# Optimization experiments

Hardware: AMD Instinct MI355X
Metric: run time of the kernel (lower is better)

The kernel has to match this reference:

```python
import jax, jax.numpy as jnp
import numpy as np

N = 100000
E = 1600000
F = 128
HID = 64
OUT = 64
LSTM_H = (3 * HID) // 2  # 96, PyG JumpingKnowledge lstm hidden size


def setup_inputs() -> dict:
    key = jax.random.key(0)
    ks = jax.random.split(key, 40)

    def w(k, shape, s=0.05):
        return jax.random.normal(k, shape, dtype=jnp.float32) * s

    inp = {}
    inp['x'] = jax.random.normal(ks[0], (N, F), dtype=jnp.float32)
    inp['edge_index'] = jax.random.randint(ks[1], (2, E), 0, N)
    # GINConv MLPs: Linear(in,hid) -> ReLU -> Linear(hid,hid)
    dims = [(F, HID), (HID, HID), (HID, HID)]
    for i, (a, b) in enumerate(dims):
        inp[f'W{i}a'] = w(ks[2 + 4 * i], (b, a))
        inp[f'b{i}a'] = w(ks[3 + 4 * i], (b,))
        inp[f'W{i}b'] = w(ks[4 + 4 * i], (b, b))
        inp[f'b{i}b'] = w(ks[5 + 4 * i], (b,))
    # JK bidirectional LSTM (torch gate order i,f,g,o)
    for j, d in enumerate(['f', 'b']):
        inp[f'Wih_{d}'] = w(ks[14 + 4 * j], (4 * LSTM_H, HID))
        inp[f'Whh_{d}'] = w(ks[15 + 4 * j], (4 * LSTM_H, LSTM_H))
        inp[f'bih_{d}'] = w(ks[16 + 4 * j], (4 * LSTM_H,))
        inp[f'bhh_{d}'] = w(ks[17 + 4 * j], (4 * LSTM_H,))
    inp['Watt'] = w(ks[22], (1, 2 * LSTM_H))
    inp['batt'] = w(ks[23], (1,))
    inp['Wlin'] = w(ks[24], (OUT, HID))
    inp['blin'] = w(ks[25], (OUT,))
    inp['Wfc1'] = w(ks[26], (1, OUT))
    inp['bfc1'] = w(ks[27], (1,))
    inp['Wfc2'] = w(ks[28], (1, N))
    inp['bfc2'] = w(ks[29], (1,))
    return inp


def _gin_layer(h, src, dst, Wa, ba, Wb, bb):
    # GINConv with eps=0: MLP((1+eps)*x + sum_{j in N(i)} x_j)
    agg = jax.ops.segment_sum(h[src], dst, num_segments=h.shape[0])
    z = h + agg
    z = jnp.maximum(z @ Wa.T + ba, 0.0)
    return z @ Wb.T + bb


def _lstm_scan(seq, Wih, Whh, bih, bhh):
    # seq: [L, N, C]; returns hidden states [L, N, H]
    H = Whh.shape[1]
    bias = bih + bhh

    def cell(carry, xt):
        hp, cp = carry
        g = xt @ Wih.T + hp @ Whh.T + bias
        i, f, gg, o = jnp.split(g, 4, axis=-1)
        c = jax.nn.sigmoid(f) * cp + jax.nn.sigmoid(i) * jnp.tanh(gg)
        hn = jax.nn.sigmoid(o) * jnp.tanh(c)
        return (hn, c), hn

    n = seq.shape[1]
    init = (jnp.zeros((n, H), seq.dtype), jnp.zeros((n, H), seq.dtype))
    _, hs = jax.lax.scan(cell, init, seq)
    return hs


def reference(x, edge_index, W0a, b0a, W0b, b0b, W1a, b1a, W1b, b1b,
              W2a, b2a, W2b, b2b, Wih_f, Whh_f, bih_f, bhh_f,
              Wih_b, Whh_b, bih_b, bhh_b, Watt, batt, Wlin, blin,
              Wfc1, bfc1, Wfc2, bfc2):
    src, dst = edge_index[0], edge_index[1]
    h = x
    xs = []
    for (Wa, ba, Wb, bb) in [(W0a, b0a, W0b, b0b), (W1a, b1a, W1b, b1b),
                             (W2a, b2a, W2b, b2b)]:
        h = _gin_layer(h, src, dst, Wa, ba, Wb, bb)
        h = jnp.maximum(h, 0.0)  # BasicGNN act (relu); dropout=identity in eval
        xs.append(h)
    seq = jnp.stack(xs, axis=0)  # [L, N, HID]
    hf = _lstm_scan(seq, Wih_f, Whh_f, bih_f, bhh_f)
    hb = _lstm_scan(seq[::-1], Wih_b, Whh_b, bih_b, bhh_b)[::-1]
    ao = jnp.concatenate([hf, hb], axis=-1)  # [L, N, 2*LSTM_H]
    alpha = (ao @ Watt.T + batt)[..., 0]  # [L, N]
    alpha = jax.nn.softmax(alpha, axis=0)  # softmax over layers
    xjk = jnp.einsum('lnc,ln->nc', seq, alpha)  # [N, HID]
    xo = xjk @ Wlin.T + blin  # [N, OUT]
    v = (xo @ Wfc1.T + bfc1)[:, 0]  # [N]
    v = jnp.where(v >= 0, v, 0.01 * v)  # LeakyReLU
    return Wfc2 @ v + bfc2  # [1]
```

## Files before the change

kernel.cpp:

```cpp
#include <hip/hip_runtime.h>
#include <stdint.h>

typedef unsigned short u16;
typedef unsigned int u32;
using short8 = __attribute__((ext_vector_type(8))) short;
using f32x16 = __attribute__((ext_vector_type(16))) float;

__device__ __forceinline__ float sigf(float x){
  return __builtin_amdgcn_rcpf(1.0f + __expf(-x));
}
__device__ __forceinline__ float tanh_f(float x){
  return 1.0f - 2.0f*__builtin_amdgcn_rcpf(1.0f + __expf(2.0f*x));
}
__device__ __forceinline__ u16 f2bf(float f){
  u32 u = __float_as_uint(f);
  u += 0x7FFFu + ((u>>16)&1u);
  return (u16)(u>>16);
}
__device__ __forceinline__ float bf2f(u16 h){ return __uint_as_float(((u32)h)<<16); }

__global__ void k_deg(const int* __restrict__ dst, int* __restrict__ deg, int E){
  int i = blockIdx.x*256 + threadIdx.x;
  if (i < E) atomicAdd(&deg[dst[i]], 1);
}

__global__ __launch_bounds__(256) void k_scan1(const int* __restrict__ deg, int* __restrict__ indptr,
                                               int* __restrict__ bsum, int N){
  __shared__ int s[256];
  int tid = threadIdx.x;
  int i = blockIdx.x*256 + tid;
  int v = (i < N) ? deg[i] : 0;
  s[tid] = v; __syncthreads();
  for (int off=1; off<256; off<<=1){
    int t = (tid>=off) ? s[tid-off] : 0;
    __syncthreads();
    s[tid] += t;
    __syncthreads();
  }
  if (i < N) indptr[i] = s[tid] - v;
  if (tid == 255) bsum[blockIdx.x] = s[255];
}

__global__ __launch_bounds__(512) void k_scan2(const int* __restrict__ bsum, int* __restrict__ boffs,
                                               int* __restrict__ indptr, int nb, int N){
  __shared__ int s[512];
  int tid = threadIdx.x;
  int v = (tid < nb) ? bsum[tid] : 0;
  s[tid] = v; __syncthreads();
  for (int off=1; off<512; off<<=1){
    int t = (tid>=off) ? s[tid-off] : 0;
    __syncthreads();
    s[tid] += t;
    __syncthreads();
  }
  boffs[tid] = s[tid] - v;
  if (tid == nb-1) indptr[N] = s[tid];
}

__global__ __launch_bounds__(256) void k_scan3(int* __restrict__ indptr, const int* __restrict__ boffs, int N){
  int i = blockIdx.x*256 + threadIdx.x;
  if (i < N) indptr[i] += boffs[blockIdx.x];
}

__global__ void k_fill(const int* __restrict__ src, const int* __restrict__ dst,
                       const int* __restrict__ indptr, int* __restrict__ fill,
                       int* __restrict__ col, int E){
  int i = blockIdx.x*256 + threadIdx.x;
  if (i < E){
    int d = dst[i];
    int r = atomicAdd(&fill[d], 1);
    col[indptr[d] + r] = src[i];
  }
}

template<int F>
__global__ __launch_bounds__(256) void k_agg(const float* __restrict__ y, const int* __restrict__ indptr,
                                             const int* __restrict__ col, const float* __restrict__ bias,
                                             float* __restrict__ z, int N){
  constexpr int TPN = F/4;
  constexpr int NPB = 256/TPN;
  int n = blockIdx.x*NPB + threadIdx.x/TPN;
  int lane = threadIdx.x % TPN;
  if (n >= N) return;
  const float4* hv = (const float4*)y;
  float4 acc = hv[(size_t)n*TPN + lane];
  int s = indptr[n], e = indptr[n+1];
  int p = s;
  for (; p + 8 <= e; p += 8){
    int c8[8];
    #pragma unroll
    for (int i=0;i<8;++i) c8[i] = col[p+i];
    #pragma unroll
    for (int i=0;i<8;++i){
      float4 x = hv[(size_t)c8[i]*TPN + lane];
      acc.x += x.x; acc.y += x.y; acc.z += x.z; acc.w += x.w;
    }
  }
  for (; p < e; ++p){
    float4 x = hv[(size_t)col[p]*TPN + lane];
    acc.x += x.x; acc.y += x.y; acc.z += x.z; acc.w += x.w;
  }
  float4 b4 = ((const float4*)bias)[lane];
  acc.x = fmaxf(acc.x + b4.x, 0.f);
  acc.y = fmaxf(acc.y + b4.y, 0.f);
  acc.z = fmaxf(acc.z + b4.z, 0.f);
  acc.w = fmaxf(acc.w + b4.w, 0.f);
  ((float4*)z)[(size_t)n*TPN + lane] = acc;
}

__device__ __forceinline__ void packW1_body(int idx, const float* __restrict__ Wih,
                                            const float* __restrict__ Whh, u16* __restrict__ Wp){
  if (idx >= 10*12*64*8) return;
  int i  = idx & 7;
  int l  = (idx>>3) & 63;
  int rt = (idx>>9) % 12;
  int kt = (idx>>9) / 12;
  int r  = rt*32 + (l & 31);
  int j  = r >> 2, g = r & 3;
  int row = g*96 + j;
  int k  = kt*16 + ((l>>5)<<3) + i;
  float v = (k < 64) ? Wih[row*64 + k] : Whh[row*96 + (k-64)];
  Wp[idx] = f2bf(v);
}

__device__ __forceinline__ void packG_body(int idx, const float* __restrict__ W,
                                           u16* __restrict__ Wg, int K){
  if (idx >= K*128) return;
  int i  = idx & 7;
  int l  = (idx>>3) & 63;
  int p  = (idx>>9) & 1;
  int rt = (idx>>10) & 1;
  int kt = idx >> 11;
  int j  = rt*32 + (l & 31);
  int k  = kt*16 + ((l>>5)<<3) + i;
  float v = W[(size_t)j*K + k];
  u16 h = f2bf(v);
  Wg[idx] = p ? f2bf(v - bf2f(h)) : h;
}

__global__ __launch_bounds__(256) void k_packAll(
    const float* __restrict__ Wih_f, const float* __restrict__ Whh_f,
    const float* __restrict__ Wih_b, const float* __restrict__ Whh_b,
    const float* __restrict__ bih_f, const float* __restrict__ bhh_f,
    const float* __restrict__ bih_b, const float* __restrict__ bhh_b,
    const float* __restrict__ W0a, const float* __restrict__ W0b,
    const float* __restrict__ W1a, const float* __restrict__ W1b,
    const float* __restrict__ W2a, const float* __restrict__ W2b,
    const float* __restrict__ Wlin,
    u16* __restrict__ Wpf, u16* __restrict__ Wpb,
    float4* __restrict__ Bpf, float4* __restrict__ Bpb,
    u16* __restrict__ Wg0a, u16* __restrict__ Wg0b,
    u16* __restrict__ Wg1a, u16* __restrict__ Wg1b,
    u16* __restrict__ Wg2a, u16* __restrict__ Wg2b,
    u16* __restrict__ WgL)
{
  int b = blockIdx.x;
  int tid = threadIdx.x;
  if (b < 240){ packW1_body(b*256+tid, Wih_f, Whh_f, Wpf); return; }
  b -= 240;
  if (b < 240){ packW1_body(b*256+tid, Wih_b, Whh_b, Wpb); return; }
  b -= 240;
  if (b == 0){
    if (tid < 96){
      int j = tid;
      Bpf[j] = make_float4(bih_f[j]+bhh_f[j], bih_f[96+j]+bhh_f[96+j],
                           bih_f[192+j]+bhh_f[192+j], bih_f[288+j]+bhh_f[288+j]);
    } else if (tid >= 128 && tid < 224){
      int j = tid - 128;
      Bpb[j] = make_float4(bih_b[j]+bhh_b[j], bih_b[96+j]+bhh_b[96+j],
                           bih_b[192+j]+bhh_b[192+j], bih_b[288+j]+bhh_b[288+j]);
    }
    return;
  }
  b -= 1;
  if (b < 64){ packG_body(b*256+tid, W0a, Wg0a, 128); return; }
  b -= 64;
  if (b < 32){ packG_body(b*256+tid, W0b, Wg0b, 64); return; }
  b -= 32;
  if (b < 32){ packG_body(b*256+tid, W1a, Wg1a, 64); return; }
  b -= 32;
  if (b < 32){ packG_body(b*256+tid, W1b, Wg1b, 64); return; }
  b -= 32;
  if (b < 32){ packG_body(b*256+tid, W2a, Wg2a, 64); return; }
  b -= 32;
  if (b < 32){ packG_body(b*256+tid, W2b, Wg2b, 64); return; }
  b -= 32;
  packG_body(b*256+tid, Wlin, WgL, 64);
}

__device__ __forceinline__ void cvt8p(const float (&v)[8], u32 (&hw)[4], u32 (&lw)[4]){
  #pragma unroll
  for (int i=0;i<4;++i){
    u16 h0=f2bf(v[2*i]),   h1=f2bf(v[2*i+1]);
    u16 l0=f2bf(v[2*i]-bf2f(h0)), l1=f2bf(v[2*i+1]-bf2f(h1));
    hw[i]= (u32)h0 | ((u32)h1<<16);
    lw[i]= (u32)l0 | ((u32)l1<<16);
  }
}

__device__ __forceinline__ void stageG(const float (&v)[8], u16* __restrict__ BH, u16* __restrict__ BL,
                                       int node, int kc, int NKT){
  u32 hw[4], lw[4];
  cvt8p(v, hw, lw);
  int kt = kc >> 1, h2 = kc & 1;
  int sl = (((h2<<5) | (node&31)) ^ (kc & 7));
  int addr = (((node>>5)*NKT + kt)<<9) + (sl<<3);
  *(uint4*)(BH + addr) = make_uint4(hw[0],hw[1],hw[2],hw[3]);
  *(uint4*)(BL + addr) = make_uint4(lw[0],lw[1],lw[2],lw[3]);
}

template<int K, int ACT>
__global__ __launch_bounds__(256,2) void k_mfgemm(const float* __restrict__ A, const u16* __restrict__ Wg,
                                                  const float* __restrict__ bias, float* __restrict__ out,
                                                  int N){
  constexpr int NKT = K/16;
  __shared__ u16 BH[2*NKT*512];
  __shared__ u16 BL[2*NKT*512];
  const int tid = threadIdx.x;
  const int l = tid & 63;
  const int w = __builtin_amdgcn_readfirstlane(tid >> 6);
  const int rt = w >> 1, nt = w & 1;
  const int nb = blockIdx.x * 64;
  const int hi = l >> 5;

  for (int u = tid; u < 64*(K/8); u += 256){
    int node = u / (K/8);
    int kc = u % (K/8);
    int n = nb + node;
    float v[8];
    if (n < N){
      const float4* s4 = (const float4*)(A + (size_t)n*K + kc*8);
      float4 a = s4[0], b = s4[1];
      v[0]=a.x; v[1]=a.y; v[2]=a.z; v[3]=a.w; v[4]=b.x; v[5]=b.y; v[6]=b.z; v[7]=b.w;
    } else {
      #pragma unroll
      for (int i=0;i<8;++i) v[i]=0.f;
    }
    stageG(v, BH, BL, node, kc, NKT);
  }
  __syncthreads();

  f32x16 acc;
  #pragma unroll
  for (int r=0;r<16;++r) acc[r] = 0.f;
  const u16* wbase = Wg + ((size_t)rt<<10) + ((size_t)l<<3);
  #pragma unroll
  for (int kt = 0; kt < NKT; ++kt){
    const u16* wk = wbase + (size_t)kt*2048;
    short8 Ah = *(const short8*)(wk);
    short8 Al = *(const short8*)(wk + 512);
    int sl = l ^ (((kt<<1) + hi) & 7);
    int baddr = ((nt*NKT + kt)<<9) + (sl<<3);
    short8 Bh = *(const short8*)(BH + baddr);
    short8 Bl = *(const short8*)(BL + baddr);
    acc = __builtin_amdgcn_mfma_f32_32x32x16_bf16(Ah, Bh, acc, 0,0,0);
    acc = __builtin_amdgcn_mfma_f32_32x32x16_bf16(Ah, Bl, acc, 0,0,0);
    acc = __builtin_amdgcn_mfma_f32_32x32x16_bf16(Al, Bh, acc, 0,0,0);
  }

  const int col = l & 31;
  const int n = nb + nt*32 + col;
  if (n < N){
    #pragma unroll
    for (int g = 0; g < 4; ++g){
      const int j0 = rt*32 + 8*g + 4*hi;
      float4 b4 = bias ? *(const float4*)(bias + j0) : make_float4(0.f,0.f,0.f,0.f);
      float4 o;
      o.x = acc[4*g+0] + b4.x;
      o.y = acc[4*g+1] + b4.y;
      o.z = acc[4*g+2] + b4.z;
      o.w = acc[4*g+3] + b4.w;
      if (ACT){
        o.x = fmaxf(o.x, 0.f); o.y = fmaxf(o.y, 0.f);
        o.z = fmaxf(o.z, 0.f); o.w = fmaxf(o.w, 0.f);
      }
      *(float4*)(out + (size_t)n*64 + j0) = o;
    }
  }
}

__global__ __launch_bounds__(256,2) void k_mfgemm2(const float* __restrict__ Z, const u16* __restrict__ Wgb,
                                                   const float* __restrict__ bb, const u16* __restrict__ Wga,
                                                   float* __restrict__ Hout, float* __restrict__ Yout,
                                                   int N){
  __shared__ u16 BH[4096];
  __shared__ u16 BL[4096];
  __shared__ float hX[64][68];
  const int tid = threadIdx.x;
  const int l = tid & 63;
  const int w = __builtin_amdgcn_readfirstlane(tid >> 6);
  const int rt = w >> 1, nt = w & 1;
  const int nb = blockIdx.x * 64;
  const int hi = l >> 5;
  const int col = l & 31;
  const int n = nb + nt*32 + col;

  for (int u = tid; u < 512; u += 256){
    int node = u >> 3;
    int kc = u & 7;
    int nn = nb + node;
    float v[8];
    if (nn < N){
      const float4* s4 = (const float4*)(Z + (size_t)nn*64 + kc*8);
      float4 a = s4[0], b = s4[1];
      v[0]=a.x; v[1]=a.y; v[2]=a.z; v[3]=a.w; v[4]=b.x; v[5]=b.y; v[6]=b.z; v[7]=b.w;
    } else {
      #pragma unroll
      for (int i=0;i<8;++i) v[i]=0.f;
    }
    stageG(v, BH, BL, node, kc, 4);
  }
  __syncthreads();

  f32x16 acc;
  #pragma unroll
  for (int r=0;r<16;++r) acc[r] = 0.f;
  {
    const u16* wbase = Wgb + ((size_t)rt<<10) + ((size_t)l<<3);
    #pragma unroll
    for (int kt = 0; kt < 4; ++kt){
      const u16* wk = wbase + (size_t)kt*2048;
      short8 Ah = *(const short8*)(wk);
      short8 Al = *(const short8*)(wk + 512);
      int sl = l ^ (((kt<<1) + hi) & 7);
      int baddr = ((nt*4 + kt)<<9) + (sl<<3);
      short8 Bh = *(const short8*)(BH + baddr);
      short8 Bl = *(const short8*)(BL + baddr);
      acc = __builtin_amdgcn_mfma_f32_32x32x16_bf16(Ah, Bh, acc, 0,0,0);
      acc = __builtin_amdgcn_mfma_f32_32x32x16_bf16(Ah, Bl, acc, 0,0,0);
      acc = __builtin_amdgcn_mfma_f32_32x32x16_bf16(Al, Bh, acc, 0,0,0);
    }
  }
  {
    const int node = nt*32 + col;
    #pragma unroll
    for (int g = 0; g < 4; ++g){
      const int j0 = rt*32 + 8*g + 4*hi;
      float4 b4 = *(const float4*)(bb + j0);
      float4 o;
      o.x = fmaxf(acc[4*g+0] + b4.x, 0.f);
      o.y = fmaxf(acc[4*g+1] + b4.y, 0.f);
      o.z = fmaxf(acc[4*g+2] + b4.z, 0.f);
      o.w = fmaxf(acc[4*g+3] + b4.w, 0.f);
      if (n < N) *(float4*)(Hout + (size_t)n*64 + j0) = o;
      *(float4*)(&hX[node][j0]) = o;
    }
  }
  __syncthreads();

  for (int u = tid; u < 512; u += 256){
    int node = u >> 3;
    int kc = u & 7;
    float v[8];
    #pragma unroll
    for (int i=0;i<8;++i) v[i] = hX[node][kc*8 + i];
    stageG(v, BH, BL, node, kc, 4);
  }
  __syncthreads();

  #pragma unroll
  for (int r=0;r<16;++r) acc[r] = 0.f;
  {
    const u16* wbase = Wga + ((size_t)rt<<10) + ((size_t)l<<3);
    #pragma unroll
    for (int kt = 0; kt < 4; ++kt){
      const u16* wk = wbase + (size_t)kt*2048;
      short8 Ah = *(const short8*)(wk);
      short8 Al = *(const short8*)(wk + 512);
      int sl = l ^ (((kt<<1) + hi) & 7);
      int baddr = ((nt*4 + kt)<<9) + (sl<<3);
      short8 Bh = *(const short8*)(BH + baddr);
      short8 Bl = *(const short8*)(BL + baddr);
      acc = __builtin_amdgcn_mfma_f32_32x32x16_bf16(Ah, Bh, acc, 0,0,0);
      acc = __builtin_amdgcn_mfma_f32_32x32x16_bf16(Ah, Bl, acc, 0,0,0);
      acc = __builtin_amdgcn_mfma_f32_32x32x16_bf16(Al, Bh, acc, 0,0,0);
    }
  }
  if (n < N){
    #pragma unroll
    for (int g = 0; g < 4; ++g){
      const int j0 = rt*32 + 8*g + 4*hi;
      float4 o;
      o.x = acc[4*g+0]; o.y = acc[4*g+1]; o.z = acc[4*g+2]; o.w = acc[4*g+3];
      *(float4*)(Yout + (size_t)n*64 + j0) = o;
    }
  }
}

__device__ __forceinline__ void ldx_regs(const float* __restrict__ seq, int blk, int N, int tid,
                                         float (&v)[8]){
  int node = tid >> 3;
  int kc = tid & 7;
  int n = blk*32 + node;
  if (n < N){
    const float4* s4 = (const float4*)(seq + (size_t)n*64 + kc*8);
    float4 a = s4[0], b = s4[1];
    v[0]=a.x; v[1]=a.y; v[2]=a.z; v[3]=a.w; v[4]=b.x; v[5]=b.y; v[6]=b.z; v[7]=b.w;
  } else {
    #pragma unroll
    for (int i=0;i<8;++i) v[i]=0.f;
  }
}

__device__ __forceinline__ void stage_x_h16(const float (&v)[8], u16* __restrict__ XH, int tid){
  int node = tid >> 3;
  int kc = tid & 7;
  u32 hw[4];
  #pragma unroll
  for (int i=0;i<4;++i)
    hw[i] = (u32)f2bf(v[2*i]) | ((u32)f2bf(v[2*i+1])<<16);
  int kt = kc >> 1, hi = kc & 1;
  int sl = (((hi<<5) | node) ^ (kc & 7));
  int addr = (kt<<9) + (sl<<3);
  *(uint4*)(XH + addr) = make_uint4(hw[0],hw[1],hw[2],hw[3]);
}

__device__ __forceinline__ void restage_h16(const u16 (*hFH)[32], u16* __restrict__ XH, int tid){
  int node = tid & 31;
  #pragma unroll
  for (int q = 0; q < 2; ++q){
    int cc = (tid >> 5) + q*8;
    if (cc < 12){
      int kth = cc >> 1, hi = cc & 1;
      int ktG = kth + 4;
      u32 hw[4];
      #pragma unroll
      for (int i=0;i<4;++i){
        u16 a = hFH[cc*8 + 2*i][node];
        u16 b = hFH[cc*8 + 2*i + 1][node];
        hw[i] = (u32)a | ((u32)b<<16);
      }
      int sl = (((hi<<5) | node) ^ ((2*ktG + hi) & 7));
      int addr = (ktG<<9) + (sl<<3);
      *(uint4*)(XH + addr) = make_uint4(hw[0],hw[1],hw[2],hw[3]);
    }
  }
}

template<int FIRST, int WRITEH>
__device__ __forceinline__ float lstm_step5(const u16* __restrict__ Wp,
    const float4* __restrict__ Bp, const float* __restrict__ WattW,
    const u16* __restrict__ XH, u16 (*hFH)[32],
    float (&c)[12], int rtg, int l)
{
  constexpr int NKT = FIRST ? 4 : 10;
  const int hi = l >> 5;
  const int col = l & 31;
  f32x16 acc[3];
  #pragma unroll
  for (int t=0;t<3;++t)
    #pragma unroll
    for (int r=0;r<16;++r) acc[t][r] = 0.f;

  const u16* wbase = Wp + (size_t)(rtg*3)*512 + ((size_t)l<<3);
  #pragma unroll
  for (int kt = 0; kt < NKT; ++kt){
    const u16* wk = wbase + (size_t)kt*6144;
    short8 A0 = *(const short8*)(wk);
    short8 A1 = *(const short8*)(wk + 512);
    short8 A2 = *(const short8*)(wk + 1024);
    int sl = l ^ (((kt<<1) + hi) & 7);
    int baddr = (kt<<9) + (sl<<3);
    short8 Bh = *(const short8*)(XH + baddr);
    __builtin_amdgcn_s_setprio(1);
    acc[0] = __builtin_amdgcn_mfma_f32_32x32x16_bf16(A0, Bh, acc[0], 0,0,0);
    acc[1] = __builtin_amdgcn_mfma_f32_32x32x16_bf16(A1, Bh, acc[1], 0,0,0);
    acc[2] = __builtin_amdgcn_mfma_f32_32x32x16_bf16(A2, Bh, acc[2], 0,0,0);
    __builtin_amdgcn_s_setprio(0);
  }

  float aP = 0.f;
  #pragma unroll
  for (int ti=0;ti<3;++ti){
    #pragma unroll
    for (int rg=0; rg<4; ++rg){
      const int j = (rtg*3+ti)*8 + 2*rg + hi;
      float4 bv = Bp[j];
      float gi = acc[ti][rg*4+0] + bv.x;
      float gf = acc[ti][rg*4+1] + bv.y;
      float gg = acc[ti][rg*4+2] + bv.z;
      float go = acc[ti][rg*4+3] + bv.w;
      const int ci = ti*4 + rg;
      float cp = FIRST ? 0.f : c[ci];
      float cn = sigf(gf)*cp + sigf(gi)*tanh_f(gg);
      float hh = sigf(go)*tanh_f(cn);
      c[ci] = cn;
      aP = fmaf(hh, WattW[j], aP);
      if (WRITEH) hFH[j][col] = f2bf(hh);
    }
  }
  return aP;
}

__global__ __launch_bounds__(256,2) void k_lstm5(
    const float* __restrict__ h1, const float* __restrict__ h2, const float* __restrict__ h3,
    const u16* __restrict__ Wpf, const u16* __restrict__ Wpb,
    const float4* __restrict__ Bpf, const float4* __restrict__ Bpb,
    const float* __restrict__ Watt, const float* __restrict__ batt,
    float* __restrict__ aF, float* __restrict__ aB, int gL, int N)
{
  __shared__ u16 XH[5120];
  __shared__ u16 hFH[96][32];
  __shared__ float sAl[4][3][32];
  const int tid = threadIdx.x;
  const int l = tid & 63;
  const int rtg = __builtin_amdgcn_readfirstlane(tid >> 6);
  const int dir = (blockIdx.x >= gL) ? 1 : 0;
  const int blk = blockIdx.x - dir*gL;
  const float* sA = dir ? h3 : h1;
  const float* sC = dir ? h1 : h3;
  const u16* Wp = dir ? Wpb : Wpf;
  const float4* Bp = dir ? Bpb : Bpf;
  const float* WattW = Watt + dir*96;
  float* aD = dir ? aB : aF;
  float c[12];
  float a0, a1, a2;
  float xv[8];

  ldx_regs(sA, blk, N, tid, xv);
  stage_x_h16(xv, XH, tid);
  ldx_regs(h2, blk, N, tid, xv);
  __syncthreads();

  a0 = lstm_step5<1,1>(Wp, Bp, WattW, XH, hFH, c, rtg, l);
  __syncthreads();
  stage_x_h16(xv, XH, tid);
  restage_h16(hFH, XH, tid);
  ldx_regs(sC, blk, N, tid, xv);
  __syncthreads();

  a1 = lstm_step5<0,1>(Wp, Bp, WattW, XH, hFH, c, rtg, l);
  __syncthreads();
  stage_x_h16(xv, XH, tid);
  restage_h16(hFH, XH, tid);
  __syncthreads();

  a2 = lstm_step5<0,0>(Wp, Bp, WattW, XH, hFH, c, rtg, l);

  a0 += __shfl_xor(a0, 32);
  a1 += __shfl_xor(a1, 32);
  a2 += __shfl_xor(a2, 32);
  if (l < 32){
    sAl[rtg][0][l] = a0;
    sAl[rtg][1][l] = a1;
    sAl[rtg][2][l] = a2;
  }
  __syncthreads();
  if (tid < 96){
    int s = tid >> 5;
    int node = tid & 31;
    int n = blk*32 + node;
    if (n < N){
      float sum = sAl[0][s][node] + sAl[1][s][node]
                + sAl[2][s][node] + sAl[3][s][node];
      int slice = dir ? (2 - s) : s;
      float v = dir ? sum : (batt[0] + sum);
      aD[(size_t)slice*N + n] = v;
    }
  }
}

__global__ __launch_bounds__(256,2) void k_jk2(const float* __restrict__ aF, const float* __restrict__ aB,
                                               const float* __restrict__ h1, const float* __restrict__ h2,
                                               const float* __restrict__ h3,
                                               const u16* __restrict__ WgL, const float* __restrict__ blin,
                                               const float* __restrict__ Wfc1, const float* __restrict__ bfc1,
                                               float* __restrict__ vout, int N){
  __shared__ u16 BH[4096];
  __shared__ u16 BL[4096];
  __shared__ float sP[4][32];
  const int tid = threadIdx.x;
  const int l = tid & 63;
  const int w = __builtin_amdgcn_readfirstlane(tid >> 6);
  const int rt = w >> 1, nt = w & 1;
  const int nb = blockIdx.x * 64;
  const int hi = l >> 5;

  for (int u = tid; u < 512; u += 256){
    int node = u >> 3;
    int kc = u & 7;
    int n = nb + node;
    float v[8];
    if (n < N){
      float a0 = aF[n] + aB[n];
      float a1 = aF[(size_t)N + n] + aB[(size_t)N + n];
      float a2 = aF[(size_t)2*N + n] + aB[(size_t)2*N + n];
      float m = fmaxf(a0, fmaxf(a1, a2));
      float e0 = __expf(a0-m), e1 = __expf(a1-m), e2 = __expf(a2-m);
      float inv = __builtin_amdgcn_rcpf(e0+e1+e2);
      float w0 = e0*inv, w1 = e1*inv, w2 = e2*inv;
      const float4* p1 = (const float4*)(h1 + (size_t)n*64 + kc*8);
      const float4* p2 = (const float4*)(h2 + (size_t)n*64 + kc*8);
      const float4* p3 = (const float4*)(h3 + (size_t)n*64 + kc*8);
      #pragma unroll
      for (int q=0;q<2;++q){
        float4 x1 = p1[q], x2 = p2[q], x3 = p3[q];
        v[4*q+0] = w0*x1.x + w1*x2.x + w2*x3.x;
        v[4*q+1] = w0*x1.y + w1*x2.y + w2*x3.y;
        v[4*q+2] = w0*x1.z + w1*x2.z + w2*x3.z;
        v[4*q+3] = w0*x1.w + w1*x2.w + w2*x3.w;
      }
    } else {
      #pragma unroll
      for (int i=0;i<8;++i) v[i]=0.f;
    }
    stageG(v, BH, BL, node, kc, 4);
  }
  __syncthreads();

  f32x16 acc;
  #pragma unroll
  for (int r=0;r<16;++r) acc[r] = 0.f;
  const u16* wbase = WgL + ((size_t)rt<<10) + ((size_t)l<<3);
  #pragma unroll
  for (int kt = 0; kt < 4; ++kt){
    const u16* wk = wbase + (size_t)kt*2048;
    short8 Ah = *(const short8*)(wk);
    short8 Al = *(const short8*)(wk + 512);
    int sl = l ^ (((kt<<1) + hi) & 7);
    int baddr = ((nt*4 + kt)<<9) + (sl<<3);
    short8 Bh = *(const short8*)(BH + baddr);
    short8 Bl = *(const short8*)(BL + baddr);
    acc = __builtin_amdgcn_mfma_f32_32x32x16_bf16(Ah, Bh, acc, 0,0,0);
    acc = __builtin_amdgcn_mfma_f32_32x32x16_bf16(Ah, Bl, acc, 0,0,0);
    acc = __builtin_amdgcn_mfma_f32_32x32x16_bf16(Al, Bh, acc, 0,0,0);
  }

  float p = 0.f;
  #pragma unroll
  for (int g = 0; g < 4; ++g){
    #pragma unroll
    for (int rg = 0; rg < 4; ++rg){
      const int j = rt*32 + 8*g + 4*hi + rg;
      p += (acc[4*g+rg] + blin[j]) * Wfc1[j];
    }
  }
  p += __shfl_xor(p, 32);
  if (l < 32) sP[w][l] = p;
  __syncthreads();
  if (tid < 64){
    int node = tid;
    int nt2 = node >> 5, c2 = node & 31;
    int n = nb + node;
    if (n < N){
      float t = sP[nt2][c2] + sP[2+nt2][c2] + bfc1[0];
      vout[n] = t >= 0.f ? t : 0.01f*t;
    }
  }
}

__global__ __launch_bounds__(256) void k_final1(const float* __restrict__ w, const float* __restrict__ v,
                                                double* __restrict__ part, int N){
  __shared__ double sd[256];
  int tid = threadIdx.x;
  double a = 0.0;
  for (int i = blockIdx.x*256 + tid; i < N; i += 256*256)
    a += (double)(w[i] * v[i]);
  sd[tid] = a; __syncthreads();
  for (int off = 128; off > 0; off >>= 1){
    if (tid < off) sd[tid] += sd[tid + off];
    __syncthreads();
  }
  if (tid == 0) part[blockIdx.x] = sd[0];
}

__global__ __launch_bounds__(256) void k_final2(const double* __restrict__ part, const float* __restrict__ bfc2,
                                                float* __restrict__ out){
  __shared__ double sd[256];
  int tid = threadIdx.x;
  sd[tid] = part[tid]; __syncthreads();
  for (int off = 128; off > 0; off >>= 1){
    if (tid < off) sd[tid] += sd[tid + off];
    __syncthreads();
  }
  if (tid == 0) out[0] = (float)(sd[0] + (double)bfc2[0]);
}

extern "C" void kernel_launch(void* const* d_in, const int* in_sizes, int n_in,
                              void* d_out, int out_size, void* d_ws, size_t ws_size,
                              hipStream_t stream){
  const float* x    = (const float*)d_in[0];
  const int*   ei   = (const int*)d_in[1];
  const float* W0a  = (const float*)d_in[2];
  const float* b0a  = (const float*)d_in[3];
  const float* W0b  = (const float*)d_in[4];
  const float* b0b  = (const float*)d_in[5];
  const float* W1a  = (const float*)d_in[6];
  const float* b1a  = (const float*)d_in[7];
  const float* W1b  = (const float*)d_in[8];
  const float* b1b  = (const float*)d_in[9];
  const float* W2a  = (const float*)d_in[10];
  const float* b2a  = (const float*)d_in[11];
  const float* W2b  = (const float*)d_in[12];
  const float* b2b  = (const float*)d_in[13];
  const float* Wih_f = (const float*)d_in[14];
  const float* Whh_f = (const float*)d_in[15];
  const float* bih_f = (const float*)d_in[16];
  const float* bhh_f = (const float*)d_in[17];
  const float* Wih_b = (const float*)d_in[18];
  const float* Whh_b = (const float*)d_in[19];
  const float* bih_b = (const float*)d_in[20];
  const float* bhh_b = (const float*)d_in[21];
  const float* Watt = (const float*)d_in[22];
  const float* batt = (const float*)d_in[23];
  const float* Wlin = (const float*)d_in[24];
  const float* blin = (const float*)d_in[25];
  const float* Wfc1 = (const float*)d_in[26];
  const float* bfc1 = (const float*)d_in[27];
  const float* Wfc2 = (const float*)d_in[28];
  const float* bfc2 = (const float*)d_in[29];
  float* out = (float*)d_out;

  const int N = in_sizes[0] / 128;
  const int E = in_sizes[1] / 2;
  const int* src = ei;
  const int* dst = ei + E;

  uint8_t* w8 = (uint8_t*)d_ws;
  size_t off = 0;
  auto alloc = [&](size_t bytes) -> void* {
    void* p = w8 + off;
    off = (off + bytes + 255) & ~(size_t)255;
    return p;
  };
  int*    deg    = (int*)   alloc((size_t)N*4);
  int*    fill   = (int*)   alloc((size_t)N*4);
  int*    indptr = (int*)   alloc(((size_t)N+1)*4);
  int*    col    = (int*)   alloc((size_t)E*4);
  int*    bsum   = (int*)   alloc(2048);
  int*    boffs  = (int*)   alloc(2048);
  float*  h1     = (float*) alloc((size_t)N*64*4);
  float*  h2     = (float*) alloc((size_t)N*64*4);
  float*  h3     = (float*) alloc((size_t)N*64*4);
  float*  aF     = (float*) alloc((size_t)3*N*4);
  float*  aB     = (float*) alloc((size_t)3*N*4);
  float*  vbuf   = (float*) alloc((size_t)N*4);
  double* part   = (double*)alloc(256*8);
  u16*    Wpf    = (u16*)   alloc((size_t)10*12*64*8*2);
  u16*    Wpb    = (u16*)   alloc((size_t)10*12*64*8*2);
  float4* Bpf    = (float4*)alloc((size_t)96*16);
  float4* Bpb    = (float4*)alloc((size_t)96*16);
  u16*    Wg0a   = (u16*)   alloc((size_t)128*128*2);
  u16*    Wg0b   = (u16*)   alloc((size_t)64*128*2);
  u16*    Wg1a   = (u16*)   alloc((size_t)64*128*2);
  u16*    Wg1b   = (u16*)   alloc((size_t)64*128*2);
  u16*    Wg2a   = (u16*)   alloc((size_t)64*128*2);
  u16*    Wg2b   = (u16*)   alloc((size_t)64*128*2);
  u16*    WgL    = (u16*)   alloc((size_t)64*128*2);
  float*  P      = (float*) alloc((size_t)N*192*4);
  if (off > ws_size) return;
  float* ybuf = P;
  float* zbuf = P + (size_t)N*64;

  size_t zlen = (size_t)((uint8_t*)fill - (uint8_t*)deg) + (size_t)N*4;
  hipMemsetAsync(deg, 0, zlen, stream);

  int gE = (E + 255) / 256;
  int nb1 = (N + 255) / 256;
  int gG = (N + 63) / 64;
  int gA = (N + 15) / 16;
  int gL = (N + 31) / 32;

  k_packAll<<<737, 256, 0, stream>>>(Wih_f, Whh_f, Wih_b, Whh_b,
                                     bih_f, bhh_f, bih_b, bhh_b,
                                     W0a, W0b, W1a, W1b, W2a, W2b, Wlin,
                                     Wpf, Wpb, Bpf, Bpb,
                                     Wg0a, Wg0b, Wg1a, Wg1b, Wg2a, Wg2b, WgL);

  k_deg  <<<gE, 256, 0, stream>>>(dst, deg, E);
  k_scan1<<<nb1, 256, 0, stream>>>(deg, indptr, bsum, N);
  k_scan2<<<1, 512, 0, stream>>>(bsum, boffs, indptr, nb1, N);
  k_scan3<<<nb1, 256, 0, stream>>>(indptr, boffs, N);
  k_fill <<<gE, 256, 0, stream>>>(src, dst, indptr, fill, col, E);

  k_mfgemm<128,0><<<gG, 256, 0, stream>>>(x, Wg0a, nullptr, ybuf, N);
  k_agg<64><<<gA, 256, 0, stream>>>(ybuf, indptr, col, b0a, zbuf, N);
  k_mfgemm2<<<gG, 256, 0, stream>>>(zbuf, Wg0b, b0b, Wg1a, h1, ybuf, N);
  k_agg<64><<<gA, 256, 0, stream>>>(ybuf, indptr, col, b1a, zbuf, N);
  k_mfgemm2<<<gG, 256, 0, stream>>>(zbuf, Wg1b, b1b, Wg2a, h2, ybuf, N);
  k_agg<64><<<gA, 256, 0, stream>>>(ybuf, indptr, col, b2a, zbuf, N);
  k_mfgemm<64,1><<<gG, 256, 0, stream>>>(zbuf, Wg2b, b2b, h3, N);

  k_lstm5<<<2*gL, 256, 0, stream>>>(h1, h2, h3, Wpf, Wpb, Bpf, Bpb, Watt, batt,
                                    aF, aB, gL, N);

  k_jk2<<<gG, 256, 0, stream>>>(aF, aB, h1, h2, h3, WgL, blin, Wfc1, bfc1, vbuf, N);

  k_final1<<<256, 256, 0, stream>>>(Wfc2, vbuf, part, N);
  k_final2<<<1, 256, 0, stream>>>(part, bfc2, out);
}
```

Baseline: 592.0 us.

## Fuse neighbor aggregation into GEMM kernels and fold final dot into JK kernel

The separate CSR aggregation kernels are merged into the following MLP GEMM kernels. Each block gathers neighbor features for its 64 nodes straight into shared memory, which drops the z buffer round trip through global memory and three launches. The final Wfc2 dot product is also folded into the JK kernel as per-block partial sums, which removes the v buffer and one reduction kernel. The LSTM launch bound is raised to 3 blocks per CU. The cost is lower gather parallelism inside the fused kernels (16 nodes per pass and fewer blocks in flight), which could hurt latency hiding for the irregular gather.

```diff
diff --git a/kernel.cpp b/kernel.cpp
--- a/kernel.cpp
+++ b/kernel.cpp
@@ -71,41 +71,6 @@
     int r = atomicAdd(&fill[d], 1);
     col[indptr[d] + r] = src[i];
   }
-}
-
-template<int F>
-__global__ __launch_bounds__(256) void k_agg(const float* __restrict__ y, const int* __restrict__ indptr,
-                                             const int* __restrict__ col, const float* __restrict__ bias,
-                                             float* __restrict__ z, int N){
-  constexpr int TPN = F/4;
-  constexpr int NPB = 256/TPN;
-  int n = blockIdx.x*NPB + threadIdx.x/TPN;
-  int lane = threadIdx.x % TPN;
-  if (n >= N) return;
-  const float4* hv = (const float4*)y;
-  float4 acc = hv[(size_t)n*TPN + lane];
-  int s = indptr[n], e = indptr[n+1];
-  int p = s;
-  for (; p + 8 <= e; p += 8){
-    int c8[8];
-    #pragma unroll
-    for (int i=0;i<8;++i) c8[i] = col[p+i];
-    #pragma unroll
-    for (int i=0;i<8;++i){
-      float4 x = hv[(size_t)c8[i]*TPN + lane];
-      acc.x += x.x; acc.y += x.y; acc.z += x.z; acc.w += x.w;
-    }
-  }
-  for (; p < e; ++p){
-    float4 x = hv[(size_t)col[p]*TPN + lane];
-    acc.x += x.x; acc.y += x.y; acc.z += x.z; acc.w += x.w;
-  }
-  float4 b4 = ((const float4*)bias)[lane];
-  acc.x = fmaxf(acc.x + b4.x, 0.f);
-  acc.y = fmaxf(acc.y + b4.y, 0.f);
-  acc.z = fmaxf(acc.z + b4.z, 0.f);
-  acc.w = fmaxf(acc.w + b4.w, 0.f);
-  ((float4*)z)[(size_t)n*TPN + lane] = acc;
 }
 
 __device__ __forceinline__ void packW1_body(int idx, const float* __restrict__ Wih,
@@ -279,10 +244,70 @@
   }
 }
 
-__global__ __launch_bounds__(256,2) void k_mfgemm2(const float* __restrict__ Z, const u16* __restrict__ Wgb,
-                                                   const float* __restrict__ bb, const u16* __restrict__ Wga,
-                                                   float* __restrict__ Hout, float* __restrict__ Yout,
-                                                   int N){
+__device__ __forceinline__ void agg_phase(const float* __restrict__ y, const int* __restrict__ indptr,
+                                          const int* __restrict__ col, const float* __restrict__ ba,
+                                          float (*hX)[68], int nb, int N, int tid){
+  const int quarter = tid & 15;
+  const int nl0 = tid >> 4;
+  const float4* hv = (const float4*)y;
+  const float4 b4 = ((const float4*)ba)[quarter];
+  #pragma unroll
+  for (int pass = 0; pass < 4; ++pass){
+    int node = pass*16 + nl0;
+    int n = nb + node;
+    float4 acc = make_float4(0.f,0.f,0.f,0.f);
+    if (n < N){
+      acc = hv[(size_t)n*16 + quarter];
+      int s = indptr[n], e = indptr[n+1];
+      int p = s;
+      for (; p + 8 <= e; p += 8){
+        int c8[8];
+        #pragma unroll
+        for (int i=0;i<8;++i) c8[i] = col[p+i];
+        #pragma unroll
+        for (int i=0;i<8;++i){
+          float4 x = hv[(size_t)c8[i]*16 + quarter];
+          acc.x += x.x; acc.y += x.y; acc.z += x.z; acc.w += x.w;
+        }
+      }
+      for (; p < e; ++p){
+        float4 x = hv[(size_t)col[p]*16 + quarter];
+        acc.x += x.x; acc.y += x.y; acc.z += x.z; acc.w += x.w;
+      }
+      acc.x = fmaxf(acc.x + b4.x, 0.f);
+      acc.y = fmaxf(acc.y + b4.y, 0.f);
+      acc.z = fmaxf(acc.z + b4.z, 0.f);
+      acc.w = fmaxf(acc.w + b4.w, 0.f);
+    }
+    *(float4*)(&hX[node][quarter<<2]) = acc;
+  }
+}
+
+__device__ __forceinline__ void gemm64(const u16* __restrict__ Wg, const u16* __restrict__ BH,
+                                       const u16* __restrict__ BL, f32x16& acc, int rt, int nt, int l){
+  const int hi = l >> 5;
+  const u16* wbase = Wg + ((size_t)rt<<10) + ((size_t)l<<3);
+  #pragma unroll
+  for (int kt = 0; kt < 4; ++kt){
+    const u16* wk = wbase + (size_t)kt*2048;
+    short8 Ah = *(const short8*)(wk);
+    short8 Al = *(const short8*)(wk + 512);
+    int sl = l ^ (((kt<<1) + hi) & 7);
+    int baddr = ((nt*4 + kt)<<9) + (sl<<3);
+    short8 Bh = *(const short8*)(BH + baddr);
+    short8 Bl = *(const short8*)(BL + baddr);
+    acc = __builtin_amdgcn_mfma_f32_32x32x16_bf16(Ah, Bh, acc, 0,0,0);
+    acc = __builtin_amdgcn_mfma_f32_32x32x16_bf16(Ah, Bl, acc, 0,0,0);
+    acc = __builtin_amdgcn_mfma_f32_32x32x16_bf16(Al, Bh, acc, 0,0,0);
+  }
+}
+
+__global__ __launch_bounds__(256,2) void k_aggGemm2(const float* __restrict__ y, const int* __restrict__ indptr,
+                                                    const int* __restrict__ col, const float* __restrict__ ba,
+                                                    const u16* __restrict__ Wgb, const float* __restrict__ bb,
+                                                    const u16* __restrict__ Wga,
+                                                    float* __restrict__ Hout, float* __restrict__ Yout,
+                                                    int N){
   __shared__ u16 BH[4096];
   __shared__ u16 BL[4096];
   __shared__ float hX[64][68];
@@ -292,22 +317,18 @@
   const int rt = w >> 1, nt = w & 1;
   const int nb = blockIdx.x * 64;
   const int hi = l >> 5;
-  const int col = l & 31;
-  const int n = nb + nt*32 + col;
+  const int cl = l & 31;
+  const int n = nb + nt*32 + cl;
+
+  agg_phase(y, indptr, col, ba, hX, nb, N, tid);
+  __syncthreads();
 
   for (int u = tid; u < 512; u += 256){
     int node = u >> 3;
     int kc = u & 7;
-    int nn = nb + node;
     float v[8];
-    if (nn < N){
-      const float4* s4 = (const float4*)(Z + (size_t)nn*64 + kc*8);
-      float4 a = s4[0], b = s4[1];
-      v[0]=a.x; v[1]=a.y; v[2]=a.z; v[3]=a.w; v[4]=b.x; v[5]=b.y; v[6]=b.z; v[7]=b.w;
-    } else {
-      #pragma unroll
-      for (int i=0;i<8;++i) v[i]=0.f;
-    }
+    #pragma unroll
+    for (int i=0;i<8;++i) v[i] = hX[node][kc*8 + i];
     stageG(v, BH, BL, node, kc, 4);
   }
   __syncthreads();
@@ -315,24 +336,9 @@
   f32x16 acc;
   #pragma unroll
   for (int r=0;r<16;++r) acc[r] = 0.f;
+  gemm64(Wgb, BH, BL, acc, rt, nt, l);
   {
-    const u16* wbase = Wgb + ((size_t)rt<<10) + ((size_t)l<<3);
-    #pragma unroll
-    for (int kt = 0; kt < 4; ++kt){
-      const u16* wk = wbase + (size_t)kt*2048;
-      short8 Ah = *(const short8*)(wk);
-      short8 Al = *(const short8*)(wk + 512);
-      int sl = l ^ (((kt<<1) + hi) & 7);
-      int baddr = ((nt*4 + kt)<<9) + (sl<<3);
-      short8 Bh = *(const short8*)(BH + baddr);
-      short8 Bl = *(const short8*)(BL + baddr);
-      acc = __builtin_amdgcn_mfma_f32_32x32x16_bf16(Ah, Bh, acc, 0,0,0);
-      acc = __builtin_amdgcn_mfma_f32_32x32x16_bf16(Ah, Bl, acc, 0,0,0);
-      acc = __builtin_amdgcn_mfma_f32_32x32x16_bf16(Al, Bh, acc, 0,0,0);
-    }
-  }
-  {
-    const int node = nt*32 + col;
+    const int node = nt*32 + cl;
     #pragma unroll
     for (int g = 0; g < 4; ++g){
       const int j0 = rt*32 + 8*g + 4*hi;
@@ -360,22 +366,7 @@
 
   #pragma unroll
   for (int r=0;r<16;++r) acc[r] = 0.f;
-  {
-    const u16* wbase = Wga + ((size_t)rt<<10) + ((size_t)l<<3);
-    #pragma unroll
-    for (int kt = 0; kt < 4; ++kt){
-      const u16* wk = wbase + (size_t)kt*2048;
-      short8 Ah = *(const short8*)(wk);
-      short8 Al = *(const short8*)(wk + 512);
-      int sl = l ^ (((kt<<1) + hi) & 7);
-      int baddr = ((nt*4 + kt)<<9) + (sl<<3);
-      short8 Bh = *(const short8*)(BH + baddr);
-      short8 Bl = *(const short8*)(BL + baddr);
-      acc = __builtin_amdgcn_mfma_f32_32x32x16_bf16(Ah, Bh, acc, 0,0,0);
-      acc = __builtin_amdgcn_mfma_f32_32x32x16_bf16(Ah, Bl, acc, 0,0,0);
-      acc = __builtin_amdgcn_mfma_f32_32x32x16_bf16(Al, Bh, acc, 0,0,0);
-    }
-  }
+  gemm64(Wga, BH, BL, acc, rt, nt, l);
   if (n < N){
     #pragma unroll
     for (int g = 0; g < 4; ++g){
@@ -383,6 +374,54 @@
       float4 o;
       o.x = acc[4*g+0]; o.y = acc[4*g+1]; o.z = acc[4*g+2]; o.w = acc[4*g+3];
       *(float4*)(Yout + (size_t)n*64 + j0) = o;
+    }
+  }
+}
+
+__global__ __launch_bounds__(256,2) void k_aggGemm1(const float* __restrict__ y, const int* __restrict__ indptr,
+                                                    const int* __restrict__ col, const float* __restrict__ ba,
+                                                    const u16* __restrict__ Wgb, const float* __restrict__ bb,
+                                                    float* __restrict__ Hout, int N){
+  __shared__ u16 BH[4096];
+  __shared__ u16 BL[4096];
+  __shared__ float hX[64][68];
+  const int tid = threadIdx.x;
+  const int l = tid & 63;
+  const int w = __builtin_amdgcn_readfirstlane(tid >> 6);
+  const int rt = w >> 1, nt = w & 1;
+  const int nb = blockIdx.x * 64;
+  const int hi = l >> 5;
+  const int cl = l & 31;
+  const int n = nb + nt*32 + cl;
+
+  agg_phase(y, indptr, col, ba, hX, nb, N, tid);
+  __syncthreads();
+
+  for (int u = tid; u < 512; u += 256){
+    int node = u >> 3;
+    int kc = u & 7;
+    float v[8];
+    #pragma unroll
+    for (int i=0;i<8;++i) v[i] = hX[node][kc*8 + i];
+    stageG(v, BH, BL, node, kc, 4);
+  }
+  __syncthreads();
+
+  f32x16 acc;
+  #pragma unroll
+  for (int r=0;r<16;++r) acc[r] = 0.f;
+  gemm64(Wgb, BH, BL, acc, rt, nt, l);
+  if (n < N){
+    #pragma unroll
+    for (int g = 0; g < 4; ++g){
+      const int j0 = rt*32 + 8*g + 4*hi;
+      float4 b4 = *(const float4*)(bb + j0);
+      float4 o;
+      o.x = fmaxf(acc[4*g+0] + b4.x, 0.f);
+      o.y = fmaxf(acc[4*g+1] + b4.y, 0.f);
+      o.z = fmaxf(acc[4*g+2] + b4.z, 0.f);
+      o.w = fmaxf(acc[4*g+3] + b4.w, 0.f);
+      *(float4*)(Hout + (size_t)n*64 + j0) = o;
     }
   }
 }
@@ -492,7 +531,7 @@
   return aP;
 }
 
-__global__ __launch_bounds__(256,2) void k_lstm5(
+__global__ __launch_bounds__(256,3) void k_lstm5(
     const float* __restrict__ h1, const float* __restrict__ h2, const float* __restrict__ h3,
     const u16* __restrict__ Wpf, const u16* __restrict__ Wpb,
     const float4* __restrict__ Bpf, const float4* __restrict__ Bpb,
@@ -565,7 +604,8 @@
                                                const float* __restrict__ h3,
                                                const u16* __restrict__ WgL, const float* __restrict__ blin,
                                                const float* __restrict__ Wfc1, const float* __restrict__ bfc1,
-                                               float* __restrict__ vout, int N){
+                                               const float* __restrict__ Wfc2,
+                                               double* __restrict__ part, int N){
   __shared__ u16 BH[4096];
   __shared__ u16 BL[4096];
   __shared__ float sP[4][32];
@@ -611,20 +651,7 @@
   f32x16 acc;
   #pragma unroll
   for (int r=0;r<16;++r) acc[r] = 0.f;
-  const u16* wbase = WgL + ((size_t)rt<<10) + ((size_t)l<<3);
-  #pragma unroll
-  for (int kt = 0; kt < 4; ++kt){
-    const u16* wk = wbase + (size_t)kt*2048;
-    short8 Ah = *(const short8*)(wk);
-    short8 Al = *(const short8*)(wk + 512);
-    int sl = l ^ (((kt<<1) + hi) & 7);
-    int baddr = ((nt*4 + kt)<<9) + (sl<<3);
-    short8 Bh = *(const short8*)(BH + baddr);
-    short8 Bl = *(const short8*)(BL + baddr);
-    acc = __builtin_amdgcn_mfma_f32_32x32x16_bf16(Ah, Bh, acc, 0,0,0);
-    acc = __builtin_amdgcn_mfma_f32_32x32x16_bf16(Ah, Bl, acc, 0,0,0);
-    acc = __builtin_amdgcn_mfma_f32_32x32x16_bf16(Al, Bh, acc, 0,0,0);
-  }
+  gemm64(WgL, BH, BL, acc, rt, nt, l);
 
   float p = 0.f;
   #pragma unroll
@@ -642,33 +669,25 @@
     int node = tid;
     int nt2 = node >> 5, c2 = node & 31;
     int n = nb + node;
+    double dv = 0.0;
     if (n < N){
       float t = sP[nt2][c2] + sP[2+nt2][c2] + bfc1[0];
-      vout[n] = t >= 0.f ? t : 0.01f*t;
-    }
-  }
-}
-
-__global__ __launch_bounds__(256) void k_final1(const float* __restrict__ w, const float* __restrict__ v,
-                                                double* __restrict__ part, int N){
+      float vv = t >= 0.f ? t : 0.01f*t;
+      dv = (double)(Wfc2[n] * vv);
+    }
+    #pragma unroll
+    for (int off = 32; off > 0; off >>= 1) dv += __shfl_down(dv, off);
+    if (tid == 0) part[blockIdx.x] = dv;
+  }
+}
+
+__global__ __launch_bounds__(256) void k_final2(const double* __restrict__ part, const float* __restrict__ bfc2,
+                                                float* __restrict__ out, int nb){
   __shared__ double sd[256];
   int tid = threadIdx.x;
   double a = 0.0;
-  for (int i = blockIdx.x*256 + tid; i < N; i += 256*256)
-    a += (double)(w[i] * v[i]);
+  for (int i = tid; i < nb; i += 256) a += part[i];
   sd[tid] = a; __syncthreads();
-  for (int off = 128; off > 0; off >>= 1){
-    if (tid < off) sd[tid] += sd[tid + off];
-    __syncthreads();
-  }
-  if (tid == 0) part[blockIdx.x] = sd[0];
-}
-
-__global__ __launch_bounds__(256) void k_final2(const double* __restrict__ part, const float* __restrict__ bfc2,
-                                                float* __restrict__ out){
-  __shared__ double sd[256];
-  int tid = threadIdx.x;
-  sd[tid] = part[tid]; __syncthreads();
   for (int off = 128; off > 0; off >>= 1){
     if (tid < off) sd[tid] += sd[tid + off];
     __syncthreads();
@@ -734,8 +753,7 @@
   float*  h3     = (float*) alloc((size_t)N*64*4);
   float*  aF     = (float*) alloc((size_t)3*N*4);
   float*  aB     = (float*) alloc((size_t)3*N*4);
-  float*  vbuf   = (float*) alloc((size_t)N*4);
-  double* part   = (double*)alloc(256*8);
+  double* part   = (double*)alloc((size_t)((N+63)/64)*8);
   u16*    Wpf    = (u16*)   alloc((size_t)10*12*64*8*2);
   u16*    Wpb    = (u16*)   alloc((size_t)10*12*64*8*2);
   float4* Bpf    = (float4*)alloc((size_t)96*16);
@@ -747,10 +765,9 @@
   u16*    Wg2a   = (u16*)   alloc((size_t)64*128*2);
   u16*    Wg2b   = (u16*)   alloc((size_t)64*128*2);
   u16*    WgL    = (u16*)   alloc((size_t)64*128*2);
-  float*  P      = (float*) alloc((size_t)N*192*4);
+  float*  yA     = (float*) alloc((size_t)N*64*4);
+  float*  yB     = (float*) alloc((size_t)N*64*4);
   if (off > ws_size) return;
-  float* ybuf = P;
-  float* zbuf = P + (size_t)N*64;
 
   size_t zlen = (size_t)((uint8_t*)fill - (uint8_t*)deg) + (size_t)N*4;
   hipMemsetAsync(deg, 0, zlen, stream);
@@ -758,7 +775,6 @@
   int gE = (E + 255) / 256;
   int nb1 = (N + 255) / 256;
   int gG = (N + 63) / 64;
-  int gA = (N + 15) / 16;
   int gL = (N + 31) / 32;
 
   k_packAll<<<737, 256, 0, stream>>>(Wih_f, Whh_f, Wih_b, Whh_b,
@@ -773,19 +789,15 @@
   k_scan3<<<nb1, 256, 0, stream>>>(indptr, boffs, N);
   k_fill <<<gE, 256, 0, stream>>>(src, dst, indptr, fill, col, E);
 
-  k_mfgemm<128,0><<<gG, 256, 0, stream>>>(x, Wg0a, nullptr, ybuf, N);
-  k_agg<64><<<gA, 256, 0, stream>>>(ybuf, indptr, col, b0a, zbuf, N);
-  k_mfgemm2<<<gG, 256, 0, stream>>>(zbuf, Wg0b, b0b, Wg1a, h1, ybuf, N);
-  k_agg<64><<<gA, 256, 0, stream>>>(ybuf, indptr, col, b1a, zbuf, N);
-  k_mfgemm2<<<gG, 256, 0, stream>>>(zbuf, Wg1b, b1b, Wg2a, h2, ybuf, N);
-  k_agg<64><<<gA, 256, 0, stream>>>(ybuf, indptr, col, b2a, zbuf, N);
-  k_mfgemm<64,1><<<gG, 256, 0, stream>>>(zbuf, Wg2b, b2b, h3, N);
+  k_mfgemm<128,0><<<gG, 256, 0, stream>>>(x, Wg0a, nullptr, yA, N);
+  k_aggGemm2<<<gG, 256, 0, stream>>>(yA, indptr, col, b0a, Wg0b, b0b, Wg1a, h1, yB, N);
+  k_aggGemm2<<<gG, 256, 0, stream>>>(yB, indptr, col, b1a, Wg1b, b1b, Wg2a, h2, yA, N);
+  k_aggGemm1<<<gG, 256, 0, stream>>>(yA, indptr, col, b2a, Wg2b, b2b, h3, N);
 
   k_lstm5<<<2*gL, 256, 0, stream>>>(h1, h2, h3, Wpf, Wpb, Bpf, Bpb, Watt, batt,
                                     aF, aB, gL, N);
 
-  k_jk2<<<gG, 256, 0, stream>>>(aF, aB, h1, h2, h3, WgL, blin, Wfc1, bfc1, vbuf, N);
-
-  k_final1<<<256, 256, 0, stream>>>(Wfc2, vbuf, part, N);
-  k_final2<<<1, 256, 0, stream>>>(part, bfc2, out);
-}
+  k_jk2<<<gG, 256, 0, stream>>>(aF, aB, h1, h2, h3, WgL, blin, Wfc1, bfc1, Wfc2, part, N);
+
+  k_final2<<<1, 256, 0, stream>>>(part, bfc2, out, gG);
+}
```

Result: no change. 598.1 us (+1.0%).
